# Optimization experiments

Hardware: AMD Instinct MI355X
Metric: run time of the kernel (lower is better)

## Reference

```python
import jax, jax.numpy as jnp
import numpy as np


def _gcn_conv(x, edge_index, edge_weight, W, b, n_nodes):
    # PyG GCNConv with normalize=True: add self-loops (weight 1), symmetric norm,
    # transform then aggregate: out[col] += norm * (x @ W)[row], plus bias.
    row = jnp.concatenate([edge_index[0], jnp.arange(n_nodes)])
    col = jnp.concatenate([edge_index[1], jnp.arange(n_nodes)])
    w = jnp.concatenate([edge_weight, jnp.ones((n_nodes,), x.dtype)])
    deg = jax.ops.segment_sum(w, col, num_segments=n_nodes)
    dinv = jnp.where(deg > 0, jax.lax.rsqrt(jnp.maximum(deg, 1e-12)), 0.0)
    norm = dinv[row] * w * dinv[col]            # [E+N]
    h = x @ W                                   # [N, out]
    msg = h[row] * norm[:, None]                # [E+N, out]
    out = jax.ops.segment_sum(msg, col, num_segments=n_nodes)
    return out + b


def setup_inputs() -> dict:
    key = jax.random.key(0)
    ks = jax.random.split(key, 6)
    N, E, F_IN, H, C = 50000, 800000, 512, 128, 40
    features = jax.random.normal(ks[0], (N, F_IN), jnp.float32)
    edge_index = jax.random.randint(ks[1], (2, E), 0, N, jnp.int64)
    edge_weight = jax.random.uniform(ks[2], (E,), jnp.float32)
    W1 = jax.random.normal(ks[3], (F_IN, H), jnp.float32) * 0.05
    b1 = jnp.zeros((H,), jnp.float32)
    W2 = jax.random.normal(ks[4], (H, C), jnp.float32) * 0.05
    b2 = jnp.zeros((C,), jnp.float32)
    return {"features": features, "edge_index": edge_index, "edge_weight": edge_weight,
            "W1": W1, "b1": b1, "W2": W2, "b2": b2}


def reference(features, edge_index, edge_weight, W1, b1, W2, b2):
    n_nodes = features.shape[0]
    x = _gcn_conv(features, edge_index, edge_weight, W1, b1, n_nodes)
    x = jax.nn.relu(x)
    # F.dropout(training=self.training): identity in eval mode
    x = _gcn_conv(x, edge_index, edge_weight, W2, b2, n_nodes)
    return jax.nn.log_softmax(x, axis=1)
```

## Files before the change

### kernel.cpp

```cpp
#include <hip/hip_runtime.h>
#include <math.h>

#define FIN  512
#define HDIM 128
#define CDIM 40
#define CPAD 48
#define CAP  64

typedef __attribute__((ext_vector_type(8))) short shortx8;
typedef __attribute__((ext_vector_type(4))) float f32x4;
typedef __attribute__((ext_vector_type(2))) float floatx2;

__device__ inline unsigned short f2bf(float x) {
    unsigned u = __builtin_bit_cast(unsigned, x);
    unsigned r = u + 0x7fffu + ((u >> 16) & 1u);
    return (unsigned short)(r >> 16);
}
__device__ inline float bfu(unsigned short v) { return __builtin_bit_cast(float, (unsigned)v << 16); }
__device__ inline float wdec(unsigned p) { return __builtin_bit_cast(float, (p & 0x7fffu) << 16); }
__device__ inline unsigned char f2fp8(float x) {
    return (unsigned char)(__builtin_amdgcn_cvt_pk_fp8_f32(x, x, 0, false) & 0xff);
}
__device__ inline floatx2 fp8x2_dec(unsigned short v) {
    return __builtin_amdgcn_cvt_pk_f32_fp8((int)(unsigned)v, false);
}

#define PREPB 280
__global__ void k_fill(const int* __restrict__ row, const int* __restrict__ col,
                       const float* __restrict__ w,
                       unsigned long long* __restrict__ cursor,
                       unsigned* __restrict__ bkt, int E, int eblocks,
                       const float* __restrict__ W1, const float* __restrict__ W2,
                       unsigned short* __restrict__ W1T, unsigned short* __restrict__ W2T) {
    if ((int)blockIdx.x >= eblocks) {
        const int i = ((int)blockIdx.x - eblocks) * 256 + (int)threadIdx.x;
        if (i < FIN * HDIM) {
            const int k = i >> 7, nn = i & 127;
            W1T[nn * FIN + k] = f2bf(W1[i]);
        } else {
            const int j = i - FIN * HDIM;
            const int nn = j >> 7, k = j & 127;
            W2T[j] = (nn < CDIM) ? f2bf(W2[k * CDIM + nn]) : (unsigned short)0;
        }
        return;
    }
    const int e = blockIdx.x * blockDim.x + threadIdx.x;
    if (e >= E) return;
    const int c = col[e];
    const float we = w[e];
    const unsigned long long wfix = (unsigned long long)(we * 4294967296.0f);
    const unsigned long long old = atomicAdd(&cursor[c], (1ULL << 40) | wfix);
    const int p = (int)(old >> 40);
    const unsigned wb = (__builtin_bit_cast(unsigned, we) + 0x8000u) >> 16;
    if (p < CAP) bkt[(size_t)c * CAP + p] = ((unsigned)row[e] << 15) | (wb & 0x7fffu);
}

__global__ void k_prep(const unsigned long long* __restrict__ cursor,
                       int* __restrict__ cnt, float* __restrict__ dinv, int n) {
    const int i = blockIdx.x * 256 + threadIdx.x;
    if (i < n) {
        const unsigned long long p = cursor[i];
        cnt[i] = min((int)(p >> 40), CAP);
        const float wsum = (float)(p & ((1ULL << 40) - 1)) * 2.3283064365386963e-10f;
        dinv[i] = rsqrtf(1.0f + wsum);
    }
}

#define G1_LDA 72
__global__ __launch_bounds__(256) void k_gemm1(const float* __restrict__ A,
                                               const unsigned short* __restrict__ W1T,
                                               const float* __restrict__ dinv,
                                               unsigned char* __restrict__ h1f8, int M) {
    __shared__ short As[64 * G1_LDA];
    __shared__ short Bs[128 * G1_LDA];
    const int tid  = threadIdx.x;
    const int wave = tid >> 6;
    const int lane = tid & 63;
    const int quad = lane >> 4;
    const int mr   = lane & 15;
    const int n0w  = wave * 32;
    const int m0b  = blockIdx.x * 64;

    const int srowA = tid >> 2, spartA = tid & 3;
    const int srowB = tid >> 1, spartB = tid & 1;

    f32x4 acc[4][2];
#pragma unroll
    for (int i = 0; i < 4; i++)
#pragma unroll
        for (int j = 0; j < 2; j++) acc[i][j] = (f32x4)0.f;

    const int growA = m0b + srowA;
    const bool okA = growA < M;
    const float* ap = A + (size_t)growA * FIN + spartA * 16;
    const unsigned short* bp = W1T + (size_t)srowB * FIN + spartB * 32;

    for (int k0 = 0; k0 < FIN; k0 += 64) {
#pragma unroll
        for (int i = 0; i < 2; i++) {
            float4 v0 = make_float4(0.f, 0.f, 0.f, 0.f), v1 = v0;
            if (okA) {
                v0 = *(const float4*)(ap + k0 + i * 8);
                v1 = *(const float4*)(ap + k0 + i * 8 + 4);
            }
            shortx8 pk;
            pk[0] = (short)f2bf(v0.x); pk[1] = (short)f2bf(v0.y);
            pk[2] = (short)f2bf(v0.z); pk[3] = (short)f2bf(v0.w);
            pk[4] = (short)f2bf(v1.x); pk[5] = (short)f2bf(v1.y);
            pk[6] = (short)f2bf(v1.z); pk[7] = (short)f2bf(v1.w);
            *(shortx8*)&As[srowA * G1_LDA + spartA * 16 + i * 8] = pk;
        }
#pragma unroll
        for (int i = 0; i < 4; i++)
            *(shortx8*)&Bs[srowB * G1_LDA + spartB * 32 + i * 8] =
                *(const shortx8*)(bp + k0 + i * 8);
        __syncthreads();

#pragma unroll
        for (int kk = 0; kk < 2; kk++) {
            shortx8 af[4], bfr[2];
#pragma unroll
            for (int mt = 0; mt < 4; mt++)
                af[mt] = *(shortx8*)&As[(mt * 16 + mr) * G1_LDA + kk * 32 + quad * 8];
#pragma unroll
            for (int nt = 0; nt < 2; nt++)
                bfr[nt] = *(shortx8*)&Bs[(n0w + nt * 16 + mr) * G1_LDA + kk * 32 + quad * 8];
#pragma unroll
            for (int mt = 0; mt < 4; mt++)
#pragma unroll
                for (int nt = 0; nt < 2; nt++)
                    acc[mt][nt] = __builtin_amdgcn_mfma_f32_16x16x32_bf16(
                        af[mt], bfr[nt], acc[mt][nt], 0, 0, 0);
        }
        __syncthreads();
    }
#pragma unroll
    for (int mt = 0; mt < 4; mt++)
#pragma unroll
        for (int r = 0; r < 4; r++) {
            const int om = m0b + mt * 16 + quad * 4 + r;
            if (om < M) {
                const float dv = dinv[om];
#pragma unroll
                for (int nt = 0; nt < 2; nt++)
                    h1f8[(size_t)om * HDIM + n0w + nt * 16 + mr] = f2fp8(dv * acc[mt][nt][r]);
            }
        }
}

#define G2_LDA 136
__global__ __launch_bounds__(1024) void k_g1g2(
    const int* __restrict__ cnt_arr, const unsigned* __restrict__ bkt,
    const unsigned char* __restrict__ h1f8,
    const float* __restrict__ dinv, const float* __restrict__ b1,
    const unsigned short* __restrict__ W2T,
    unsigned short* __restrict__ h2a, unsigned short* __restrict__ h2b,
    int n_nodes) {
    __shared__ short Xs[16 * G2_LDA];
    const int tid  = threadIdx.x;
    const int wave = tid >> 6;
    const int lane = tid & 63;
    const int loff = lane * 2;
    const int m0b  = blockIdx.x * 16;
    const int node = m0b + wave;

    unsigned val = 0u;
    if (node < n_nodes) {
        const int cnt = cnt_arr[node];
        const unsigned* base = bkt + (size_t)node * CAP;
        float a0 = 0.f, a1 = 0.f, c0 = 0.f, c1 = 0.f;
        int s = 0;
        for (; s + 8 <= cnt; s += 8) {
            const uint4 qa = *(const uint4*)(base + s);
            const uint4 qb = *(const uint4*)(base + s + 4);
            const unsigned short v0 = *(const unsigned short*)(h1f8 + (size_t)(qa.x >> 15) * HDIM + loff);
            const unsigned short v1 = *(const unsigned short*)(h1f8 + (size_t)(qa.y >> 15) * HDIM + loff);
            const unsigned short v2 = *(const unsigned short*)(h1f8 + (size_t)(qa.z >> 15) * HDIM + loff);
            const unsigned short v3 = *(const unsigned short*)(h1f8 + (size_t)(qa.w >> 15) * HDIM + loff);
            const unsigned short v4 = *(const unsigned short*)(h1f8 + (size_t)(qb.x >> 15) * HDIM + loff);
            const unsigned short v5 = *(const unsigned short*)(h1f8 + (size_t)(qb.y >> 15) * HDIM + loff);
            const unsigned short v6 = *(const unsigned short*)(h1f8 + (size_t)(qb.z >> 15) * HDIM + loff);
            const unsigned short v7 = *(const unsigned short*)(h1f8 + (size_t)(qb.w >> 15) * HDIM + loff);
            const floatx2 f0 = fp8x2_dec(v0), f1 = fp8x2_dec(v1), f2 = fp8x2_dec(v2), f3 = fp8x2_dec(v3);
            const floatx2 f4 = fp8x2_dec(v4), f5 = fp8x2_dec(v5), f6 = fp8x2_dec(v6), f7 = fp8x2_dec(v7);
            a0 += wdec(qa.x) * f0.x + wdec(qa.y) * f1.x + wdec(qa.z) * f2.x + wdec(qa.w) * f3.x;
            a1 += wdec(qa.x) * f0.y + wdec(qa.y) * f1.y + wdec(qa.z) * f2.y + wdec(qa.w) * f3.y;
            c0 += wdec(qb.x) * f4.x + wdec(qb.y) * f5.x + wdec(qb.z) * f6.x + wdec(qb.w) * f7.x;
            c1 += wdec(qb.x) * f4.y + wdec(qb.y) * f5.y + wdec(qb.z) * f6.y + wdec(qb.w) * f7.y;
        }
        for (; s + 4 <= cnt; s += 4) {
            const uint4 qa = *(const uint4*)(base + s);
            const unsigned short v0 = *(const unsigned short*)(h1f8 + (size_t)(qa.x >> 15) * HDIM + loff);
            const unsigned short v1 = *(const unsigned short*)(h1f8 + (size_t)(qa.y >> 15) * HDIM + loff);
            const unsigned short v2 = *(const unsigned short*)(h1f8 + (size_t)(qa.z >> 15) * HDIM + loff);
            const unsigned short v3 = *(const unsigned short*)(h1f8 + (size_t)(qa.w >> 15) * HDIM + loff);
            const floatx2 f0 = fp8x2_dec(v0), f1 = fp8x2_dec(v1), f2 = fp8x2_dec(v2), f3 = fp8x2_dec(v3);
            a0 += wdec(qa.x) * f0.x + wdec(qa.y) * f1.x + wdec(qa.z) * f2.x + wdec(qa.w) * f3.x;
            a1 += wdec(qa.x) * f0.y + wdec(qa.y) * f1.y + wdec(qa.z) * f2.y + wdec(qa.w) * f3.y;
        }
        for (; s < cnt; s++) {
            const unsigned p = base[s];
            const unsigned short v = *(const unsigned short*)(h1f8 + (size_t)(p >> 15) * HDIM + loff);
            const floatx2 f = fp8x2_dec(v);
            a0 += wdec(p) * f.x;
            a1 += wdec(p) * f.y;
        }
        a0 += c0; a1 += c1;
        const float dl = dinv[node];
        const unsigned short vs = *(const unsigned short*)(h1f8 + (size_t)node * HDIM + loff);
        const floatx2 fs = fp8x2_dec(vs);
        a0 = fmaxf(dl * (a0 + fs.x) + b1[loff], 0.f);
        a1 = fmaxf(dl * (a1 + fs.y) + b1[loff + 1], 0.f);
        val = (unsigned)f2bf(a0) | ((unsigned)f2bf(a1) << 16);
    }
    *(unsigned*)&Xs[wave * G2_LDA + loff] = val;
    __syncthreads();

    if (wave < 3) {
        const int quad = lane >> 4;
        const int mr   = lane & 15;
        const int nt   = wave;
        f32x4 acc = (f32x4)0.f;
#pragma unroll
        for (int kk = 0; kk < 4; kk++) {
            const shortx8 af  = *(const shortx8*)&Xs[mr * G2_LDA + kk * 32 + quad * 8];
            const shortx8 bfr = *(const shortx8*)(W2T + (size_t)(nt * 16 + mr) * HDIM + kk * 32 + quad * 8);
            acc = __builtin_amdgcn_mfma_f32_16x16x32_bf16(af, bfr, acc, 0, 0, 0);
        }
#pragma unroll
        for (int r = 0; r < 4; r++) {
            const int om = m0b + quad * 4 + r;
            if (om < n_nodes) {
                const float dv = dinv[om];
                if (nt < 2)       h2a[(size_t)om * 32 + nt * 16 + mr] = f2bf(dv * acc[r]);
                else if (mr < 8)  h2b[(size_t)om * 8 + mr] = f2bf(dv * acc[r]);
            }
        }
    }
}

__global__ __launch_bounds__(256) void k_gather2(
    const int* __restrict__ cnt_arr, const unsigned* __restrict__ bkt,
    const unsigned short* __restrict__ h2a, const unsigned short* __restrict__ h2b,
    const float* __restrict__ dinv, const float* __restrict__ b2,
    float* __restrict__ out, int n_nodes) {
    const int node = blockIdx.x * 4 + (threadIdx.x >> 6);
    const int lane = threadIdx.x & 63;
    if (node >= n_nodes) return;
    const bool act = lane < CDIM;
    const int cnt = cnt_arr[node];
    const unsigned* base = bkt + (size_t)node * CAP;
    const unsigned short* hb = (lane < 32) ? (h2a + lane) : (h2b + (lane & 7));
    const int hstride = (lane < 32) ? 32 : 8;
    float acc = 0.f, accb = 0.f;
    int s = 0;
    for (; s + 4 <= cnt; s += 4) {
        const uint4 q = *(const uint4*)(base + s);
        if (act) {
            acc  += wdec(q.x) * bfu(hb[(size_t)(q.x >> 15) * hstride])
                  + wdec(q.y) * bfu(hb[(size_t)(q.y >> 15) * hstride]);
            accb += wdec(q.z) * bfu(hb[(size_t)(q.z >> 15) * hstride])
                  + wdec(q.w) * bfu(hb[(size_t)(q.w >> 15) * hstride]);
        }
    }
    for (; s < cnt; s++) {
        const unsigned p = base[s];
        if (act) acc += wdec(p) * bfu(hb[(size_t)(p >> 15) * hstride]);
    }
    acc += accb;
    if (act) {
        const float dl = dinv[node];
        acc = dl * (acc + bfu(hb[(size_t)node * hstride])) + b2[lane];
    }
    float m = act ? acc : -INFINITY;
#pragma unroll
    for (int off = 32; off; off >>= 1) m = fmaxf(m, __shfl_xor(m, off));
    float se = act ? expf(acc - m) : 0.f;
#pragma unroll
    for (int off = 32; off; off >>= 1) se += __shfl_xor(se, off);
    if (act) out[(size_t)node * CDIM + lane] = acc - m - logf(se);
}

extern "C" void kernel_launch(void* const* d_in, const int* in_sizes, int n_in,
                              void* d_out, int out_size, void* d_ws, size_t ws_size,
                              hipStream_t stream) {
    const float* features = (const float*)d_in[0];
    const int*   eidx     = (const int*)d_in[1];
    const float* ew       = (const float*)d_in[2];
    const float* W1       = (const float*)d_in[3];
    const float* b1       = (const float*)d_in[4];
    const float* W2       = (const float*)d_in[5];
    const float* b2       = (const float*)d_in[6];
    float* out = (float*)d_out;

    const int Nn = in_sizes[0] / FIN;
    const int E  = in_sizes[2];
    const int* row = eidx;
    const int* col = eidx + E;

    char* ws = (char*)d_ws;
    size_t off = 0;
    auto alloc = [&](size_t bytes) { void* p = ws + off; off += (bytes + 255) & ~(size_t)255; return p; };
    unsigned long long* cursor = (unsigned long long*)alloc((size_t)Nn * 8);
    int*      cnt          = (int*)     alloc((size_t)Nn * 4);
    float*    dinv         = (float*)   alloc((size_t)Nn * 4);
    unsigned* bkt          = (unsigned*)alloc((size_t)Nn * CAP * 4);
    unsigned short* W1T    = (unsigned short*)alloc((size_t)FIN * HDIM * 2);
    unsigned short* W2T    = (unsigned short*)alloc((size_t)CPAD * HDIM * 2);
    unsigned char*  h1f8   = (unsigned char*) alloc((size_t)Nn * HDIM);
    unsigned short* h2a    = (unsigned short*)alloc((size_t)Nn * 32 * 2);
    unsigned short* h2b    = (unsigned short*)alloc((size_t)Nn * 8 * 2);

    const int eblocks = (E + 255) / 256;

    hipMemsetAsync(cursor, 0, (size_t)Nn * 8, stream);
    k_fill<<<eblocks + PREPB, 256, 0, stream>>>(row, col, ew, cursor, bkt, E, eblocks,
                                                W1, W2, W1T, W2T);
    k_prep<<<(Nn + 255) / 256, 256, 0, stream>>>(cursor, cnt, dinv, Nn);
    k_gemm1<<<(Nn + 63) / 64, 256, 0, stream>>>(features, W1T, dinv, h1f8, Nn);
    k_g1g2<<<(Nn + 15) / 16, 1024, 0, stream>>>(cnt, bkt, h1f8, dinv, b1, W2T,
                                                h2a, h2b, Nn);
    k_gather2<<<(Nn + 3) / 4, 256, 0, stream>>>(cnt, bkt, h2a, h2b, dinv, b2, out, Nn);
}
```

Measured before the change: 313.9 us.

## Drop prep kernel, enlarge GEMM1 tile, replace layer-2 MFMA with per-node dot

Removes the k_prep kernel by decoding count and inverse degree directly from the packed cursor in every consumer kernel. Enlarges the first GEMM tile to 128x128 per block with a 2x2 wave split so each wave computes 64x64, raising MFMA work per loaded tile. Restructures the fused aggregation+layer-2 kernel to 256-thread blocks of 4 nodes, staging W2 in shared memory and computing the 40-wide projection with scalar bf16 dot products instead of a 16-node MFMA. This trades one launch and the cnt/dinv arrays for repeated rsqrt work, and changes occupancy and the W2 staging cost per block.

```diff
diff --git a/kernel.cpp b/kernel.cpp
--- a/kernel.cpp
+++ b/kernel.cpp
@@ -17,12 +17,18 @@
     return (unsigned short)(r >> 16);
 }
 __device__ inline float bfu(unsigned short v) { return __builtin_bit_cast(float, (unsigned)v << 16); }
+__device__ inline float bflo(unsigned u) { return __builtin_bit_cast(float, u << 16); }
+__device__ inline float bfhi(unsigned u) { return __builtin_bit_cast(float, u & 0xffff0000u); }
 __device__ inline float wdec(unsigned p) { return __builtin_bit_cast(float, (p & 0x7fffu) << 16); }
 __device__ inline unsigned char f2fp8(float x) {
     return (unsigned char)(__builtin_amdgcn_cvt_pk_fp8_f32(x, x, 0, false) & 0xff);
 }
 __device__ inline floatx2 fp8x2_dec(unsigned short v) {
     return __builtin_amdgcn_cvt_pk_f32_fp8((int)(unsigned)v, false);
+}
+__device__ inline int cur_cnt(unsigned long long p) { return min((int)(p >> 40), CAP); }
+__device__ inline float cur_dinv(unsigned long long p) {
+    return rsqrtf(1.0f + (float)(p & ((1ULL << 40) - 1)) * 2.3283064365386963e-10f);
 }
 
 #define PREPB 280
@@ -55,51 +61,41 @@
     if (p < CAP) bkt[(size_t)c * CAP + p] = ((unsigned)row[e] << 15) | (wb & 0x7fffu);
 }
 
-__global__ void k_prep(const unsigned long long* __restrict__ cursor,
-                       int* __restrict__ cnt, float* __restrict__ dinv, int n) {
-    const int i = blockIdx.x * 256 + threadIdx.x;
-    if (i < n) {
-        const unsigned long long p = cursor[i];
-        cnt[i] = min((int)(p >> 40), CAP);
-        const float wsum = (float)(p & ((1ULL << 40) - 1)) * 2.3283064365386963e-10f;
-        dinv[i] = rsqrtf(1.0f + wsum);
-    }
-}
-
 #define G1_LDA 72
 __global__ __launch_bounds__(256) void k_gemm1(const float* __restrict__ A,
                                                const unsigned short* __restrict__ W1T,
-                                               const float* __restrict__ dinv,
+                                               const unsigned long long* __restrict__ cursor,
                                                unsigned char* __restrict__ h1f8, int M) {
-    __shared__ short As[64 * G1_LDA];
+    __shared__ short As[128 * G1_LDA];
     __shared__ short Bs[128 * G1_LDA];
     const int tid  = threadIdx.x;
     const int wave = tid >> 6;
     const int lane = tid & 63;
     const int quad = lane >> 4;
     const int mr   = lane & 15;
-    const int n0w  = wave * 32;
-    const int m0b  = blockIdx.x * 64;
-
-    const int srowA = tid >> 2, spartA = tid & 3;
-    const int srowB = tid >> 1, spartB = tid & 1;
-
-    f32x4 acc[4][2];
+    const int m0w  = (wave & 1) * 64;
+    const int n0w  = (wave >> 1) * 64;
+    const int m0b  = blockIdx.x * 128;
+
+    const int srow = tid >> 1;
+    const int spart = tid & 1;
+
+    f32x4 acc[4][4];
 #pragma unroll
     for (int i = 0; i < 4; i++)
 #pragma unroll
-        for (int j = 0; j < 2; j++) acc[i][j] = (f32x4)0.f;
-
-    const int growA = m0b + srowA;
-    const bool okA = growA < M;
-    const float* ap = A + (size_t)growA * FIN + spartA * 16;
-    const unsigned short* bp = W1T + (size_t)srowB * FIN + spartB * 32;
+        for (int j = 0; j < 4; j++) acc[i][j] = (f32x4)0.f;
+
+    const int grow = m0b + srow;
+    const bool arow_ok = grow < M;
+    const float* ap = A + (size_t)grow * FIN + spart * 32;
+    const unsigned short* bp = W1T + (size_t)srow * FIN + spart * 32;
 
     for (int k0 = 0; k0 < FIN; k0 += 64) {
 #pragma unroll
-        for (int i = 0; i < 2; i++) {
+        for (int i = 0; i < 4; i++) {
             float4 v0 = make_float4(0.f, 0.f, 0.f, 0.f), v1 = v0;
-            if (okA) {
+            if (arow_ok) {
                 v0 = *(const float4*)(ap + k0 + i * 8);
                 v1 = *(const float4*)(ap + k0 + i * 8 + 4);
             }
@@ -108,27 +104,27 @@
             pk[2] = (short)f2bf(v0.z); pk[3] = (short)f2bf(v0.w);
             pk[4] = (short)f2bf(v1.x); pk[5] = (short)f2bf(v1.y);
             pk[6] = (short)f2bf(v1.z); pk[7] = (short)f2bf(v1.w);
-            *(shortx8*)&As[srowA * G1_LDA + spartA * 16 + i * 8] = pk;
+            *(shortx8*)&As[srow * G1_LDA + spart * 32 + i * 8] = pk;
         }
 #pragma unroll
         for (int i = 0; i < 4; i++)
-            *(shortx8*)&Bs[srowB * G1_LDA + spartB * 32 + i * 8] =
+            *(shortx8*)&Bs[srow * G1_LDA + spart * 32 + i * 8] =
                 *(const shortx8*)(bp + k0 + i * 8);
         __syncthreads();
 
 #pragma unroll
         for (int kk = 0; kk < 2; kk++) {
-            shortx8 af[4], bfr[2];
+            shortx8 af[4], bfr[4];
 #pragma unroll
             for (int mt = 0; mt < 4; mt++)
-                af[mt] = *(shortx8*)&As[(mt * 16 + mr) * G1_LDA + kk * 32 + quad * 8];
-#pragma unroll
-            for (int nt = 0; nt < 2; nt++)
+                af[mt] = *(shortx8*)&As[(m0w + mt * 16 + mr) * G1_LDA + kk * 32 + quad * 8];
+#pragma unroll
+            for (int nt = 0; nt < 4; nt++)
                 bfr[nt] = *(shortx8*)&Bs[(n0w + nt * 16 + mr) * G1_LDA + kk * 32 + quad * 8];
 #pragma unroll
             for (int mt = 0; mt < 4; mt++)
 #pragma unroll
-                for (int nt = 0; nt < 2; nt++)
+                for (int nt = 0; nt < 4; nt++)
                     acc[mt][nt] = __builtin_amdgcn_mfma_f32_16x16x32_bf16(
                         af[mt], bfr[nt], acc[mt][nt], 0, 0, 0);
         }
@@ -138,117 +134,117 @@
     for (int mt = 0; mt < 4; mt++)
 #pragma unroll
         for (int r = 0; r < 4; r++) {
-            const int om = m0b + mt * 16 + quad * 4 + r;
+            const int om = m0b + m0w + mt * 16 + quad * 4 + r;
             if (om < M) {
-                const float dv = dinv[om];
-#pragma unroll
-                for (int nt = 0; nt < 2; nt++)
+                const float dv = cur_dinv(cursor[om]);
+#pragma unroll
+                for (int nt = 0; nt < 4; nt++)
                     h1f8[(size_t)om * HDIM + n0w + nt * 16 + mr] = f2fp8(dv * acc[mt][nt][r]);
             }
         }
 }
 
-#define G2_LDA 136
-__global__ __launch_bounds__(1024) void k_g1g2(
-    const int* __restrict__ cnt_arr, const unsigned* __restrict__ bkt,
+#define W2LD 130
+__global__ __launch_bounds__(256) void k_g1g2(
+    const unsigned long long* __restrict__ cursor, const unsigned* __restrict__ bkt,
     const unsigned char* __restrict__ h1f8,
-    const float* __restrict__ dinv, const float* __restrict__ b1,
+    const float* __restrict__ b1,
     const unsigned short* __restrict__ W2T,
     unsigned short* __restrict__ h2a, unsigned short* __restrict__ h2b,
     int n_nodes) {
-    __shared__ short Xs[16 * G2_LDA];
+    __shared__ unsigned short W2s[CPAD * W2LD];
+    __shared__ unsigned short Xs[4 * 128];
     const int tid  = threadIdx.x;
     const int wave = tid >> 6;
     const int lane = tid & 63;
     const int loff = lane * 2;
-    const int m0b  = blockIdx.x * 16;
-    const int node = m0b + wave;
-
-    unsigned val = 0u;
-    if (node < n_nodes) {
-        const int cnt = cnt_arr[node];
-        const unsigned* base = bkt + (size_t)node * CAP;
-        float a0 = 0.f, a1 = 0.f, c0 = 0.f, c1 = 0.f;
-        int s = 0;
-        for (; s + 8 <= cnt; s += 8) {
-            const uint4 qa = *(const uint4*)(base + s);
-            const uint4 qb = *(const uint4*)(base + s + 4);
-            const unsigned short v0 = *(const unsigned short*)(h1f8 + (size_t)(qa.x >> 15) * HDIM + loff);
-            const unsigned short v1 = *(const unsigned short*)(h1f8 + (size_t)(qa.y >> 15) * HDIM + loff);
-            const unsigned short v2 = *(const unsigned short*)(h1f8 + (size_t)(qa.z >> 15) * HDIM + loff);
-            const unsigned short v3 = *(const unsigned short*)(h1f8 + (size_t)(qa.w >> 15) * HDIM + loff);
-            const unsigned short v4 = *(const unsigned short*)(h1f8 + (size_t)(qb.x >> 15) * HDIM + loff);
-            const unsigned short v5 = *(const unsigned short*)(h1f8 + (size_t)(qb.y >> 15) * HDIM + loff);
-            const unsigned short v6 = *(const unsigned short*)(h1f8 + (size_t)(qb.z >> 15) * HDIM + loff);
-            const unsigned short v7 = *(const unsigned short*)(h1f8 + (size_t)(qb.w >> 15) * HDIM + loff);
-            const floatx2 f0 = fp8x2_dec(v0), f1 = fp8x2_dec(v1), f2 = fp8x2_dec(v2), f3 = fp8x2_dec(v3);
-            const floatx2 f4 = fp8x2_dec(v4), f5 = fp8x2_dec(v5), f6 = fp8x2_dec(v6), f7 = fp8x2_dec(v7);
-            a0 += wdec(qa.x) * f0.x + wdec(qa.y) * f1.x + wdec(qa.z) * f2.x + wdec(qa.w) * f3.x;
-            a1 += wdec(qa.x) * f0.y + wdec(qa.y) * f1.y + wdec(qa.z) * f2.y + wdec(qa.w) * f3.y;
-            c0 += wdec(qb.x) * f4.x + wdec(qb.y) * f5.x + wdec(qb.z) * f6.x + wdec(qb.w) * f7.x;
-            c1 += wdec(qb.x) * f4.y + wdec(qb.y) * f5.y + wdec(qb.z) * f6.y + wdec(qb.w) * f7.y;
-        }
-        for (; s + 4 <= cnt; s += 4) {
-            const uint4 qa = *(const uint4*)(base + s);
-            const unsigned short v0 = *(const unsigned short*)(h1f8 + (size_t)(qa.x >> 15) * HDIM + loff);
-            const unsigned short v1 = *(const unsigned short*)(h1f8 + (size_t)(qa.y >> 15) * HDIM + loff);
-            const unsigned short v2 = *(const unsigned short*)(h1f8 + (size_t)(qa.z >> 15) * HDIM + loff);
-            const unsigned short v3 = *(const unsigned short*)(h1f8 + (size_t)(qa.w >> 15) * HDIM + loff);
-            const floatx2 f0 = fp8x2_dec(v0), f1 = fp8x2_dec(v1), f2 = fp8x2_dec(v2), f3 = fp8x2_dec(v3);
-            a0 += wdec(qa.x) * f0.x + wdec(qa.y) * f1.x + wdec(qa.z) * f2.x + wdec(qa.w) * f3.x;
-            a1 += wdec(qa.x) * f0.y + wdec(qa.y) * f1.y + wdec(qa.z) * f2.y + wdec(qa.w) * f3.y;
-        }
-        for (; s < cnt; s++) {
-            const unsigned p = base[s];
-            const unsigned short v = *(const unsigned short*)(h1f8 + (size_t)(p >> 15) * HDIM + loff);
-            const floatx2 f = fp8x2_dec(v);
-            a0 += wdec(p) * f.x;
-            a1 += wdec(p) * f.y;
-        }
-        a0 += c0; a1 += c1;
-        const float dl = dinv[node];
-        const unsigned short vs = *(const unsigned short*)(h1f8 + (size_t)node * HDIM + loff);
-        const floatx2 fs = fp8x2_dec(vs);
-        a0 = fmaxf(dl * (a0 + fs.x) + b1[loff], 0.f);
-        a1 = fmaxf(dl * (a1 + fs.y) + b1[loff + 1], 0.f);
-        val = (unsigned)f2bf(a0) | ((unsigned)f2bf(a1) << 16);
-    }
-    *(unsigned*)&Xs[wave * G2_LDA + loff] = val;
+
+    for (int i = tid; i < CPAD * (HDIM / 8); i += 256) {
+        const int r = i >> 4, j = (i & 15) * 8;
+        *(shortx8*)&W2s[r * W2LD + j] = *(const shortx8*)(W2T + r * HDIM + j);
+    }
     __syncthreads();
 
-    if (wave < 3) {
-        const int quad = lane >> 4;
-        const int mr   = lane & 15;
-        const int nt   = wave;
-        f32x4 acc = (f32x4)0.f;
-#pragma unroll
-        for (int kk = 0; kk < 4; kk++) {
-            const shortx8 af  = *(const shortx8*)&Xs[mr * G2_LDA + kk * 32 + quad * 8];
-            const shortx8 bfr = *(const shortx8*)(W2T + (size_t)(nt * 16 + mr) * HDIM + kk * 32 + quad * 8);
-            acc = __builtin_amdgcn_mfma_f32_16x16x32_bf16(af, bfr, acc, 0, 0, 0);
-        }
-#pragma unroll
-        for (int r = 0; r < 4; r++) {
-            const int om = m0b + quad * 4 + r;
-            if (om < n_nodes) {
-                const float dv = dinv[om];
-                if (nt < 2)       h2a[(size_t)om * 32 + nt * 16 + mr] = f2bf(dv * acc[r]);
-                else if (mr < 8)  h2b[(size_t)om * 8 + mr] = f2bf(dv * acc[r]);
-            }
-        }
+    const int node = blockIdx.x * 4 + wave;
+    if (node >= n_nodes) return;
+    const unsigned long long cp = cursor[node];
+    const int cnt = cur_cnt(cp);
+    const float dl = cur_dinv(cp);
+    const unsigned* base = bkt + (size_t)node * CAP;
+    float a0 = 0.f, a1 = 0.f, c0 = 0.f, c1 = 0.f;
+    int s = 0;
+    for (; s + 8 <= cnt; s += 8) {
+        const uint4 qa = *(const uint4*)(base + s);
+        const uint4 qb = *(const uint4*)(base + s + 4);
+        const unsigned short v0 = *(const unsigned short*)(h1f8 + (size_t)(qa.x >> 15) * HDIM + loff);
+        const unsigned short v1 = *(const unsigned short*)(h1f8 + (size_t)(qa.y >> 15) * HDIM + loff);
+        const unsigned short v2 = *(const unsigned short*)(h1f8 + (size_t)(qa.z >> 15) * HDIM + loff);
+        const unsigned short v3 = *(const unsigned short*)(h1f8 + (size_t)(qa.w >> 15) * HDIM + loff);
+        const unsigned short v4 = *(const unsigned short*)(h1f8 + (size_t)(qb.x >> 15) * HDIM + loff);
+        const unsigned short v5 = *(const unsigned short*)(h1f8 + (size_t)(qb.y >> 15) * HDIM + loff);
+        const unsigned short v6 = *(const unsigned short*)(h1f8 + (size_t)(qb.z >> 15) * HDIM + loff);
+        const unsigned short v7 = *(const unsigned short*)(h1f8 + (size_t)(qb.w >> 15) * HDIM + loff);
+        const floatx2 f0 = fp8x2_dec(v0), f1 = fp8x2_dec(v1), f2 = fp8x2_dec(v2), f3 = fp8x2_dec(v3);
+        const floatx2 f4 = fp8x2_dec(v4), f5 = fp8x2_dec(v5), f6 = fp8x2_dec(v6), f7 = fp8x2_dec(v7);
+        a0 += wdec(qa.x) * f0.x + wdec(qa.y) * f1.x + wdec(qa.z) * f2.x + wdec(qa.w) * f3.x;
+        a1 += wdec(qa.x) * f0.y + wdec(qa.y) * f1.y + wdec(qa.z) * f2.y + wdec(qa.w) * f3.y;
+        c0 += wdec(qb.x) * f4.x + wdec(qb.y) * f5.x + wdec(qb.z) * f6.x + wdec(qb.w) * f7.x;
+        c1 += wdec(qb.x) * f4.y + wdec(qb.y) * f5.y + wdec(qb.z) * f6.y + wdec(qb.w) * f7.y;
+    }
+    for (; s + 4 <= cnt; s += 4) {
+        const uint4 qa = *(const uint4*)(base + s);
+        const unsigned short v0 = *(const unsigned short*)(h1f8 + (size_t)(qa.x >> 15) * HDIM + loff);
+        const unsigned short v1 = *(const unsigned short*)(h1f8 + (size_t)(qa.y >> 15) * HDIM + loff);
+        const unsigned short v2 = *(const unsigned short*)(h1f8 + (size_t)(qa.z >> 15) * HDIM + loff);
+        const unsigned short v3 = *(const unsigned short*)(h1f8 + (size_t)(qa.w >> 15) * HDIM + loff);
+        const floatx2 f0 = fp8x2_dec(v0), f1 = fp8x2_dec(v1), f2 = fp8x2_dec(v2), f3 = fp8x2_dec(v3);
+        a0 += wdec(qa.x) * f0.x + wdec(qa.y) * f1.x + wdec(qa.z) * f2.x + wdec(qa.w) * f3.x;
+        a1 += wdec(qa.x) * f0.y + wdec(qa.y) * f1.y + wdec(qa.z) * f2.y + wdec(qa.w) * f3.y;
+    }
+    for (; s < cnt; s++) {
+        const unsigned p = base[s];
+        const unsigned short v = *(const unsigned short*)(h1f8 + (size_t)(p >> 15) * HDIM + loff);
+        const floatx2 f = fp8x2_dec(v);
+        a0 += wdec(p) * f.x;
+        a1 += wdec(p) * f.y;
+    }
+    a0 += c0; a1 += c1;
+    const unsigned short vs = *(const unsigned short*)(h1f8 + (size_t)node * HDIM + loff);
+    const floatx2 fs = fp8x2_dec(vs);
+    a0 = fmaxf(dl * (a0 + fs.x) + b1[loff], 0.f);
+    a1 = fmaxf(dl * (a1 + fs.y) + b1[loff + 1], 0.f);
+    *(unsigned*)&Xs[wave * 128 + loff] = (unsigned)f2bf(a0) | ((unsigned)f2bf(a1) << 16);
+
+    if (lane < CDIM) {
+        float acc = 0.f;
+#pragma unroll
+        for (int j = 0; j < 16; j++) {
+            const shortx8 xv = *(const shortx8*)&Xs[wave * 128 + j * 8];
+            const shortx8 wv = *(const shortx8*)&W2s[lane * W2LD + j * 8];
+            const unsigned* xu = (const unsigned*)&xv;
+            const unsigned* wu = (const unsigned*)&wv;
+#pragma unroll
+            for (int p = 0; p < 4; p++)
+                acc += bflo(xu[p]) * bflo(wu[p]) + bfhi(xu[p]) * bfhi(wu[p]);
+        }
+        const unsigned short hv = f2bf(dl * acc);
+        if (lane < 32) h2a[(size_t)node * 32 + lane] = hv;
+        else           h2b[(size_t)node * 8 + (lane - 32)] = hv;
     }
 }
 
 __global__ __launch_bounds__(256) void k_gather2(
-    const int* __restrict__ cnt_arr, const unsigned* __restrict__ bkt,
+    const unsigned long long* __restrict__ cursor, const unsigned* __restrict__ bkt,
     const unsigned short* __restrict__ h2a, const unsigned short* __restrict__ h2b,
-    const float* __restrict__ dinv, const float* __restrict__ b2,
+    const float* __restrict__ b2,
     float* __restrict__ out, int n_nodes) {
     const int node = blockIdx.x * 4 + (threadIdx.x >> 6);
     const int lane = threadIdx.x & 63;
     if (node >= n_nodes) return;
     const bool act = lane < CDIM;
-    const int cnt = cnt_arr[node];
+    const unsigned long long cp = cursor[node];
+    const int cnt = cur_cnt(cp);
+    const float dl = cur_dinv(cp);
     const unsigned* base = bkt + (size_t)node * CAP;
     const unsigned short* hb = (lane < 32) ? (h2a + lane) : (h2b + (lane & 7));
     const int hstride = (lane < 32) ? 32 : 8;
@@ -268,10 +264,7 @@
         if (act) acc += wdec(p) * bfu(hb[(size_t)(p >> 15) * hstride]);
     }
     acc += accb;
-    if (act) {
-        const float dl = dinv[node];
-        acc = dl * (acc + bfu(hb[(size_t)node * hstride])) + b2[lane];
-    }
+    if (act) acc = dl * (acc + bfu(hb[(size_t)node * hstride])) + b2[lane];
     float m = act ? acc : -INFINITY;
 #pragma unroll
     for (int off = 32; off; off >>= 1) m = fmaxf(m, __shfl_xor(m, off));
@@ -302,8 +295,6 @@
     size_t off = 0;
     auto alloc = [&](size_t bytes) { void* p = ws + off; off += (bytes + 255) & ~(size_t)255; return p; };
     unsigned long long* cursor = (unsigned long long*)alloc((size_t)Nn * 8);
-    int*      cnt          = (int*)     alloc((size_t)Nn * 4);
-    float*    dinv         = (float*)   alloc((size_t)Nn * 4);
     unsigned* bkt          = (unsigned*)alloc((size_t)Nn * CAP * 4);
     unsigned short* W1T    = (unsigned short*)alloc((size_t)FIN * HDIM * 2);
     unsigned short* W2T    = (unsigned short*)alloc((size_t)CPAD * HDIM * 2);
@@ -316,9 +307,7 @@
     hipMemsetAsync(cursor, 0, (size_t)Nn * 8, stream);
     k_fill<<<eblocks + PREPB, 256, 0, stream>>>(row, col, ew, cursor, bkt, E, eblocks,
                                                 W1, W2, W1T, W2T);
-    k_prep<<<(Nn + 255) / 256, 256, 0, stream>>>(cursor, cnt, dinv, Nn);
-    k_gemm1<<<(Nn + 63) / 64, 256, 0, stream>>>(features, W1T, dinv, h1f8, Nn);
-    k_g1g2<<<(Nn + 15) / 16, 1024, 0, stream>>>(cnt, bkt, h1f8, dinv, b1, W2T,
-                                                h2a, h2b, Nn);
-    k_gather2<<<(Nn + 3) / 4, 256, 0, stream>>>(cnt, bkt, h2a, h2b, dinv, b2, out, Nn);
-}
+    k_gemm1<<<(Nn + 127) / 128, 256, 0, stream>>>(features, W1T, cursor, h1f8, Nn);
+    k_g1g2<<<(Nn + 3) / 4, 256, 0, stream>>>(cursor, bkt, h1f8, b1, W2T, h2a, h2b, Nn);
+    k_gather2<<<(Nn + 3) / 4, 256, 0, stream>>>(cursor, bkt, h2a, h2b, b2, out, Nn);
+}
```

New measurement: 318.3 us. Within noise of the previous version (+1.4%).
